# Kernel tuning notes

Hardware: AMD Instinct MI355X
Metric: run time of the kernel (lower is better)

## Reference

```python
import jax, jax.numpy as jnp
import numpy as np

B, M, N_DIM = 2048, 1024, 64


def setup_inputs() -> dict:
    key = jax.random.key(0)
    ks = jax.random.split(key, 6)
    X = jax.random.normal(ks[0], (B, N_DIM), dtype=jnp.float32)
    Mu0 = jax.random.normal(ks[1], (M, N_DIM), dtype=jnp.float32)
    Mu1 = jax.random.normal(ks[2], (M, N_DIM), dtype=jnp.float32)
    # diagonal variances must be positive
    S0 = jax.random.uniform(ks[3], (M, N_DIM), dtype=jnp.float32, minval=0.1, maxval=1.0)
    S1 = jax.random.uniform(ks[4], (M, N_DIM), dtype=jnp.float32, minval=0.1, maxval=1.0)
    Lam = jax.random.uniform(ks[5], (M,), dtype=jnp.float32, minval=0.01, maxval=1.0)
    Lam = Lam / jnp.sum(Lam)  # transport-plan weights sum to 1
    return {"X": X, "Mu0": Mu0, "Mu1": Mu1, "S0": S0, "S1": S1,
            "Lam": Lam, "t": 0.3, "epsilon": 0.5}


def reference(X, Mu0, Mu1, S0, S1, Lam, t, epsilon):
    # GMMflow_fast.calc_u with sparse coupling of M nonzero (i,j) pairs.
    eps2 = epsilon ** 2
    Ds = jnp.sqrt(4.0 * S0 * S1 + epsilon ** 4)            # [M, n]
    Cs = 0.5 * (Ds - eps2)                                  # [M, n]
    v = Mu1 - Mu0                                           # [M, n]
    Mut = (1.0 - t) * Mu0 + t * Mu1                         # [M, n]
    Sigma = ((1.0 - t) ** 2) * S0 + (t ** 2) * S1 + 2.0 * t * (1.0 - t) * (Cs + 0.5 * eps2)
    Pt = t * S1 + (1.0 - t) * Cs
    Qt = (1.0 - t) * S0 + t * Cs
    St = Pt - Qt - eps2 * t
    K = St / Sigma                                          # [M, n]

    Xd = X[:, None, :] - Mut[None, :, :]                    # [B, M, n]
    U = K[None, :, :] * Xd + v[None, :, :]                  # [B, M, n]

    # Gaussian log-prob plus (n/2) log(2*pi), matching the torch code:
    # log N(x; mu, Sigma) + n/2 log(2pi) = -0.5 * sum(d^2/Sigma + log Sigma)
    logw = -0.5 * jnp.sum(Xd * Xd / Sigma[None, :, :] + jnp.log(Sigma)[None, :, :], axis=-1)  # [B, M]
    logw = jnp.clip(logw, -50.0, 50.0)
    W = jnp.exp(logw) * Lam[None, :]                        # [B, M]

    u = jnp.einsum('bm,bmd->bd', W, U)                      # [B, n]
    norm = jnp.sum(W, axis=1, keepdims=True)                # [B, 1]
    return u / norm
```

## Files before the change

kernel.cpp:

```cpp
#include <hip/hip_runtime.h>
#include <math.h>


#define B_N 2048
#define M_N 1024
#define NSPLIT 16
#define BT 64
#define MS 64
#define PROW 132

typedef short bf16x8 __attribute__((ext_vector_type(8)));
typedef float f32x4 __attribute__((ext_vector_type(4)));

static __device__ __forceinline__ unsigned short bf16rn(float f) {
    union { float f; unsigned u; } v; v.f = f;
    unsigned r = v.u + 0x7FFF + ((v.u >> 16) & 1);
    return (unsigned short)(r >> 16);
}
static __device__ __forceinline__ float bf2f(unsigned short h) {
    union { unsigned u; float f; } v; v.u = ((unsigned)h) << 16;
    return v.f;
}
static __device__ __forceinline__ void st4(unsigned short* p, unsigned short a,
                                           unsigned short b, unsigned short c, unsigned short d) {
    union { unsigned short u[4]; float2 f; } t;
    t.u[0] = a; t.u[1] = b; t.u[2] = c; t.u[3] = d;
    *(float2*)p = t.f;
}

__global__ __launch_bounds__(256)
void prep_kernel(const float* __restrict__ Mu0, const float* __restrict__ Mu1,
                 const float* __restrict__ S0, const float* __restrict__ S1,
                 const float* __restrict__ T, const float* __restrict__ E,
                 unsigned short* __restrict__ B1h, unsigned short* __restrict__ B1l,
                 unsigned short* __restrict__ VTh, float* __restrict__ qArr) {
    __shared__ float sK[16 * 65];
    __shared__ float sG[16 * 65];
    const int tid = threadIdx.x;
    const int m0 = blockIdx.x * 16;
    const float t = T[0], e = E[0];
    const float eps2 = e * e, eps4 = eps2 * eps2, omt = 1.f - t;
    const int d = tid & 63;
    #pragma unroll
    for (int it = 0; it < 4; it++) {
        int mi = it * 4 + (tid >> 6);
        int m = m0 + mi;
        int idx = m * 64 + d;
        float s0 = S0[idx], s1 = S1[idx];
        float mu0 = Mu0[idx], mu1 = Mu1[idx];
        float Ds = sqrtf(4.f * s0 * s1 + eps4);
        float Cs = 0.5f * (Ds - eps2);
        float sig = omt * omt * s0 + t * t * s1 + 2.f * t * omt * (Cs + 0.5f * eps2);
        float St = (t * s1 + omt * Cs) - (omt * s0 + t * Cs) - eps2 * t;
        float a = 1.f / sig;
        float K = St * a;
        float mut = omt * mu0 + t * mu1;
        float pp = -2.f * mut * a;
        float g = (mu1 - mu0) - K * mut;
        unsigned short ah = bf16rn(a);
        B1h[m * 128 + d] = ah;
        B1l[m * 128 + d] = bf16rn(a - bf2f(ah));
        unsigned short ph = bf16rn(pp);
        B1h[m * 128 + 64 + d] = ph;
        B1l[m * 128 + 64 + d] = bf16rn(pp - bf2f(ph));
        sK[mi * 65 + d] = K;
        sG[mi * 65 + d] = g;
        float qd = mut * mut * a + logf(sig);
        #pragma unroll
        for (int off = 32; off > 0; off >>= 1) qd += __shfl_xor(qd, off, 64);
        if (d == 0) qArr[m] = qd;
    }
    __syncthreads();
    #pragma unroll
    for (int it = 0; it < 8; it++) {
        int i = it * 256 + tid;
        int n = i >> 4, mm = i & 15;
        float v = (n < 64) ? sK[mm * 65 + n] : sG[mm * 65 + (n - 64)];
        VTh[n * M_N + m0 + mm] = bf16rn(v);
    }
}

__global__ __launch_bounds__(256, 2)
void gmm_main_kernel(const float* __restrict__ X, const float* __restrict__ Lam,
                     const unsigned short* __restrict__ B1h, const unsigned short* __restrict__ B1l,
                     const unsigned short* __restrict__ VTh,
                     const float* __restrict__ qArr, float* __restrict__ part) {
    __shared__ __align__(16) char smem_raw[70144];
    unsigned short* sm = (unsigned short*)smem_raw;
    unsigned short* sA1h = sm;
    unsigned short* sA1l = sm + 8704;
    unsigned short* sB1h = sm + 17408;
    unsigned short* sB1l = sm + 26112;
    unsigned short* sV   = sm;
    unsigned short* sW   = sm + 17408;
    float* sQ = (float*)(smem_raw + 69632);
    float* sL = (float*)(smem_raw + 69888);

    const int tid  = threadIdx.x;
    const int Boff = blockIdx.x * BT;
    const int Moff = blockIdx.y * MS;
    const int w    = tid >> 6;
    const int lane = tid & 63;
    const int c = lane & 15, q = lane >> 4;
    const int wb = w >> 1;
    const int wm = w & 1;

    {
        const float4* X4 = (const float4*)X;
        #pragma unroll
        for (int it = 0; it < 4; it++) {
            int i = it * 256 + tid;
            int b = i >> 4, dq = i & 15;
            float4 xv = X4[(size_t)(Boff + b) * 16 + dq];
            float xs[4] = {xv.x, xv.y, xv.z, xv.w};
            unsigned short yh[4], yl[4], xh[4], xl[4];
            #pragma unroll
            for (int k = 0; k < 4; k++) {
                float y = xs[k] * xs[k];
                yh[k] = bf16rn(y);  yl[k] = bf16rn(y - bf2f(yh[k]));
                xh[k] = bf16rn(xs[k]);  xl[k] = bf16rn(xs[k] - bf2f(xh[k]));
            }
            int base = b * 136 + 4 * dq;
            st4(sA1h + base, yh[0], yh[1], yh[2], yh[3]);
            st4(sA1l + base, yl[0], yl[1], yl[2], yl[3]);
            st4(sA1h + base + 64, xh[0], xh[1], xh[2], xh[3]);
            st4(sA1l + base + 64, xl[0], xl[1], xl[2], xl[3]);
        }
        const float4* gBh = (const float4*)B1h + (size_t)Moff * 16;
        const float4* gBl = (const float4*)B1l + (size_t)Moff * 16;
        #pragma unroll
        for (int it = 0; it < 4; it++) {
            int i = it * 256 + tid;
            int row = i >> 4, cc = i & 15;
            *(float4*)(sB1h + row * 136 + cc * 8) = gBh[row * 16 + cc];
            *(float4*)(sB1l + row * 136 + cc * 8) = gBl[row * 16 + cc];
        }
        if (tid < 64) sQ[tid] = qArr[Moff + tid];
        else if (tid < 128) sL[tid - 64] = Lam[Moff + tid - 64];
    }
    __syncthreads();

    f32x4 acc1[2][2];
    #pragma unroll
    for (int i = 0; i < 2; i++)
        #pragma unroll
        for (int j = 0; j < 2; j++) acc1[i][j] = (f32x4){0.f, 0.f, 0.f, 0.f};
    #pragma unroll
    for (int ks = 0; ks < 4; ks++) {
        bf16x8 Ah[2], Al[2], Bh[2], Bl[2];
        #pragma unroll
        for (int i = 0; i < 2; i++) {
            int row = wb * 32 + i * 16 + c;
            Ah[i] = *(const bf16x8*)(sA1h + row * 136 + ks * 32 + q * 8);
            Al[i] = *(const bf16x8*)(sA1l + row * 136 + ks * 32 + q * 8);
        }
        #pragma unroll
        for (int j = 0; j < 2; j++) {
            int row = wm * 32 + j * 16 + c;
            Bh[j] = *(const bf16x8*)(sB1h + row * 136 + ks * 32 + q * 8);
            Bl[j] = *(const bf16x8*)(sB1l + row * 136 + ks * 32 + q * 8);
        }
        #pragma unroll
        for (int i = 0; i < 2; i++)
            #pragma unroll
            for (int j = 0; j < 2; j++) {
                acc1[i][j] = __builtin_amdgcn_mfma_f32_16x16x32_bf16(Ah[i], Bh[j], acc1[i][j], 0, 0, 0);
                acc1[i][j] = __builtin_amdgcn_mfma_f32_16x16x32_bf16(Ah[i], Bl[j], acc1[i][j], 0, 0, 0);
                acc1[i][j] = __builtin_amdgcn_mfma_f32_16x16x32_bf16(Al[i], Bh[j], acc1[i][j], 0, 0, 0);
            }
    }
    __syncthreads();

    {
        const float4* gV = (const float4*)VTh;
        int mo8 = Moff >> 3;
        #pragma unroll
        for (int it = 0; it < 4; it++) {
            int i = it * 256 + tid;
            int row = i >> 3, cc = i & 7;
            *(float4*)(sV + row * 72 + cc * 8) = gV[(size_t)row * 128 + mo8 + cc];
        }
        float nsum[2][4];
        #pragma unroll
        for (int i = 0; i < 2; i++)
            #pragma unroll
            for (int r = 0; r < 4; r++) nsum[i][r] = 0.f;
        #pragma unroll
        for (int i = 0; i < 2; i++)
            #pragma unroll
            for (int j = 0; j < 2; j++) {
                int m = wm * 32 + j * 16 + c;
                float qm = sQ[m], lm = sL[m];
                #pragma unroll
                for (int r = 0; r < 4; r++) {
                    int bl = wb * 32 + i * 16 + q * 4 + r;
                    float lw = -0.5f * (acc1[i][j][r] + qm);
                    lw = fminf(50.f, fmaxf(-50.f, lw));
                    float wf = __expf(lw) * lm;
                    unsigned short wh = bf16rn(wf);
                    sW[bl * 72 + m] = wh;
                    nsum[i][r] += bf2f(wh);
                }
            }
        #pragma unroll
        for (int mask = 1; mask <= 8; mask <<= 1)
            #pragma unroll
            for (int i = 0; i < 2; i++)
                #pragma unroll
                for (int r = 0; r < 4; r++)
                    nsum[i][r] += __shfl_xor(nsum[i][r], mask, 64);
        if (c == 0) {
            #pragma unroll
            for (int i = 0; i < 2; i++)
                #pragma unroll
                for (int r = 0; r < 4; r++) {
                    int b = Boff + wb * 32 + i * 16 + q * 4 + r;
                    part[((size_t)blockIdx.y * B_N + b) * PROW + 128 + wm] = nsum[i][r];
                }
        }
    }
    __syncthreads();

    f32x4 acc2[2][4];
    #pragma unroll
    for (int i = 0; i < 2; i++)
        #pragma unroll
        for (int j = 0; j < 4; j++) acc2[i][j] = (f32x4){0.f, 0.f, 0.f, 0.f};
    #pragma unroll
    for (int ks = 0; ks < 2; ks++) {
        bf16x8 Wf[2], Vf[4];
        #pragma unroll
        for (int i = 0; i < 2; i++) {
            int row = wb * 32 + i * 16 + c;
            Wf[i] = *(const bf16x8*)(sW + row * 72 + ks * 32 + q * 8);
        }
        #pragma unroll
        for (int j = 0; j < 4; j++) {
            int row = wm * 64 + j * 16 + c;
            Vf[j] = *(const bf16x8*)(sV + row * 72 + ks * 32 + q * 8);
        }
        #pragma unroll
        for (int i = 0; i < 2; i++)
            #pragma unroll
            for (int j = 0; j < 4; j++)
                acc2[i][j] = __builtin_amdgcn_mfma_f32_16x16x32_bf16(Wf[i], Vf[j], acc2[i][j], 0, 0, 0);
    }

    #pragma unroll
    for (int i = 0; i < 2; i++)
        #pragma unroll
        for (int j = 0; j < 4; j++) {
            #pragma unroll
            for (int r = 0; r < 4; r++) {
                int b = Boff + wb * 32 + i * 16 + q * 4 + r;
                int n = wm * 64 + j * 16 + c;
                part[((size_t)blockIdx.y * B_N + b) * PROW + n] = acc2[i][j][r];
            }
        }
}

__global__ __launch_bounds__(256)
void finalize_kernel(const float* __restrict__ X, const float* __restrict__ part,
                     float* __restrict__ out) {
    int gid = blockIdx.x * 256 + threadIdx.x;
    int b = gid >> 6, d = gid & 63;
    float a1 = 0.f, a2 = 0.f, nn = 0.f;
    #pragma unroll
    for (int s = 0; s < NSPLIT; s++) {
        const float* row = part + ((size_t)s * B_N + b) * PROW;
        a1 += row[d];
        a2 += row[64 + d];
        nn += row[128] + row[129];
    }
    out[gid] = (X[gid] * a1 + a2) / nn;
}

extern "C" void kernel_launch(void* const* d_in, const int* in_sizes, int n_in,
                              void* d_out, int out_size, void* d_ws, size_t ws_size,
                              hipStream_t stream) {
    (void)in_sizes; (void)n_in; (void)out_size; (void)ws_size;
    const float* X   = (const float*)d_in[0];
    const float* Mu0 = (const float*)d_in[1];
    const float* Mu1 = (const float*)d_in[2];
    const float* S0  = (const float*)d_in[3];
    const float* S1  = (const float*)d_in[4];
    const float* Lam = (const float*)d_in[5];
    const float* T   = (const float*)d_in[6];
    const float* E   = (const float*)d_in[7];

    char* ws = (char*)d_ws;
    unsigned short* B1h = (unsigned short*)(ws);
    unsigned short* B1l = (unsigned short*)(ws + 262144);
    unsigned short* VTh = (unsigned short*)(ws + 524288);
    float* qArr = (float*)(ws + 786432);
    float* part = (float*)(ws + 790528);

    prep_kernel<<<64, 256, 0, stream>>>(Mu0, Mu1, S0, S1, T, E, B1h, B1l, VTh, qArr);
    dim3 grid(B_N / BT, NSPLIT);
    gmm_main_kernel<<<grid, 256, 0, stream>>>(X, Lam, B1h, B1l, VTh, qArr, part);
    finalize_kernel<<<512, 256, 0, stream>>>(X, part, (float*)d_out);
}
```

Baseline: 90.08 us.

## Fuse prep and finalize into main kernel with last-block reduction

The separate prep kernel is removed: each main-kernel block now recomputes its slice of per-component coefficients (B1 hi/lo, K/g, q) directly into shared memory and registers. The finalize kernel is also removed. Instead, an atomic counter per batch tile lets the last-arriving split block sum the partials and write the output. This cuts two launches and the global round trips for the intermediates. In exchange, coefficient work is repeated across the 32 batch tiles, register pressure rises from the kg array, and a memset plus atomics are added.

```diff
diff --git a/kernel.cpp b/kernel.cpp
--- a/kernel.cpp
+++ b/kernel.cpp
@@ -28,64 +28,15 @@
     *(float2*)p = t.f;
 }
 
-__global__ __launch_bounds__(256)
-void prep_kernel(const float* __restrict__ Mu0, const float* __restrict__ Mu1,
-                 const float* __restrict__ S0, const float* __restrict__ S1,
-                 const float* __restrict__ T, const float* __restrict__ E,
-                 unsigned short* __restrict__ B1h, unsigned short* __restrict__ B1l,
-                 unsigned short* __restrict__ VTh, float* __restrict__ qArr) {
-    __shared__ float sK[16 * 65];
-    __shared__ float sG[16 * 65];
-    const int tid = threadIdx.x;
-    const int m0 = blockIdx.x * 16;
-    const float t = T[0], e = E[0];
-    const float eps2 = e * e, eps4 = eps2 * eps2, omt = 1.f - t;
-    const int d = tid & 63;
-    #pragma unroll
-    for (int it = 0; it < 4; it++) {
-        int mi = it * 4 + (tid >> 6);
-        int m = m0 + mi;
-        int idx = m * 64 + d;
-        float s0 = S0[idx], s1 = S1[idx];
-        float mu0 = Mu0[idx], mu1 = Mu1[idx];
-        float Ds = sqrtf(4.f * s0 * s1 + eps4);
-        float Cs = 0.5f * (Ds - eps2);
-        float sig = omt * omt * s0 + t * t * s1 + 2.f * t * omt * (Cs + 0.5f * eps2);
-        float St = (t * s1 + omt * Cs) - (omt * s0 + t * Cs) - eps2 * t;
-        float a = 1.f / sig;
-        float K = St * a;
-        float mut = omt * mu0 + t * mu1;
-        float pp = -2.f * mut * a;
-        float g = (mu1 - mu0) - K * mut;
-        unsigned short ah = bf16rn(a);
-        B1h[m * 128 + d] = ah;
-        B1l[m * 128 + d] = bf16rn(a - bf2f(ah));
-        unsigned short ph = bf16rn(pp);
-        B1h[m * 128 + 64 + d] = ph;
-        B1l[m * 128 + 64 + d] = bf16rn(pp - bf2f(ph));
-        sK[mi * 65 + d] = K;
-        sG[mi * 65 + d] = g;
-        float qd = mut * mut * a + logf(sig);
-        #pragma unroll
-        for (int off = 32; off > 0; off >>= 1) qd += __shfl_xor(qd, off, 64);
-        if (d == 0) qArr[m] = qd;
-    }
-    __syncthreads();
-    #pragma unroll
-    for (int it = 0; it < 8; it++) {
-        int i = it * 256 + tid;
-        int n = i >> 4, mm = i & 15;
-        float v = (n < 64) ? sK[mm * 65 + n] : sG[mm * 65 + (n - 64)];
-        VTh[n * M_N + m0 + mm] = bf16rn(v);
-    }
-}
-
 __global__ __launch_bounds__(256, 2)
-void gmm_main_kernel(const float* __restrict__ X, const float* __restrict__ Lam,
-                     const unsigned short* __restrict__ B1h, const unsigned short* __restrict__ B1l,
-                     const unsigned short* __restrict__ VTh,
-                     const float* __restrict__ qArr, float* __restrict__ part) {
-    __shared__ __align__(16) char smem_raw[70144];
+void gmm_main_kernel(const float* __restrict__ X,
+                     const float* __restrict__ Mu0, const float* __restrict__ Mu1,
+                     const float* __restrict__ S0, const float* __restrict__ S1,
+                     const float* __restrict__ Lam,
+                     const float* __restrict__ T, const float* __restrict__ E,
+                     float* __restrict__ part, int* __restrict__ cnt,
+                     float* __restrict__ out) {
+    __shared__ __align__(16) char smem_raw[70400];
     unsigned short* sm = (unsigned short*)smem_raw;
     unsigned short* sA1h = sm;
     unsigned short* sA1l = sm + 8704;
@@ -95,6 +46,7 @@
     unsigned short* sW   = sm + 17408;
     float* sQ = (float*)(smem_raw + 69632);
     float* sL = (float*)(smem_raw + 69888);
+    int*  sWin = (int*)(smem_raw + 70144);
 
     const int tid  = threadIdx.x;
     const int Boff = blockIdx.x * BT;
@@ -104,14 +56,49 @@
     const int c = lane & 15, q = lane >> 4;
     const int wb = w >> 1;
     const int wm = w & 1;
-
+    const int d  = lane;
+    const int mq = tid >> 6;
+
+    ushort2 kg[16];
+    {
+        const float t = T[0], e = E[0];
+        const float eps2 = e * e, eps4 = eps2 * eps2, omt = 1.f - t;
+        #pragma unroll 4
+        for (int it = 0; it < 16; it++) {
+            int mloc = it * 4 + mq;
+            int idx = (Moff + mloc) * 64 + d;
+            float s0 = S0[idx], s1 = S1[idx];
+            float mu0 = Mu0[idx], mu1 = Mu1[idx];
+            float Ds = sqrtf(4.f * s0 * s1 + eps4);
+            float Cs = 0.5f * (Ds - eps2);
+            float sig = omt * omt * s0 + t * t * s1 + 2.f * t * omt * (Cs + 0.5f * eps2);
+            float St = (t * s1 + omt * Cs) - (omt * s0 + t * Cs) - eps2 * t;
+            float a = 1.f / sig;
+            float K = St * a;
+            float mut = omt * mu0 + t * mu1;
+            float pp = -2.f * mut * a;
+            float g = (mu1 - mu0) - K * mut;
+            unsigned short ah = bf16rn(a);
+            sB1h[mloc * 136 + d] = ah;
+            sB1l[mloc * 136 + d] = bf16rn(a - bf2f(ah));
+            unsigned short ph = bf16rn(pp);
+            sB1h[mloc * 136 + 64 + d] = ph;
+            sB1l[mloc * 136 + 64 + d] = bf16rn(pp - bf2f(ph));
+            kg[it] = make_ushort2(bf16rn(K), bf16rn(g));
+            float qd = mut * mut * a + __logf(sig);
+            #pragma unroll
+            for (int off = 32; off > 0; off >>= 1) qd += __shfl_xor(qd, off, 64);
+            if (d == 0) sQ[mloc] = qd;
+        }
+        if (tid < 64) sL[tid] = Lam[Moff + tid];
+    }
     {
         const float4* X4 = (const float4*)X;
         #pragma unroll
         for (int it = 0; it < 4; it++) {
             int i = it * 256 + tid;
-            int b = i >> 4, dq = i & 15;
-            float4 xv = X4[(size_t)(Boff + b) * 16 + dq];
+            int b = i >> 4, dq4 = i & 15;
+            float4 xv = X4[(size_t)(Boff + b) * 16 + dq4];
             float xs[4] = {xv.x, xv.y, xv.z, xv.w};
             unsigned short yh[4], yl[4], xh[4], xl[4];
             #pragma unroll
@@ -120,23 +107,12 @@
                 yh[k] = bf16rn(y);  yl[k] = bf16rn(y - bf2f(yh[k]));
                 xh[k] = bf16rn(xs[k]);  xl[k] = bf16rn(xs[k] - bf2f(xh[k]));
             }
-            int base = b * 136 + 4 * dq;
+            int base = b * 136 + 4 * dq4;
             st4(sA1h + base, yh[0], yh[1], yh[2], yh[3]);
             st4(sA1l + base, yl[0], yl[1], yl[2], yl[3]);
             st4(sA1h + base + 64, xh[0], xh[1], xh[2], xh[3]);
             st4(sA1l + base + 64, xl[0], xl[1], xl[2], xl[3]);
         }
-        const float4* gBh = (const float4*)B1h + (size_t)Moff * 16;
-        const float4* gBl = (const float4*)B1l + (size_t)Moff * 16;
-        #pragma unroll
-        for (int it = 0; it < 4; it++) {
-            int i = it * 256 + tid;
-            int row = i >> 4, cc = i & 15;
-            *(float4*)(sB1h + row * 136 + cc * 8) = gBh[row * 16 + cc];
-            *(float4*)(sB1l + row * 136 + cc * 8) = gBl[row * 16 + cc];
-        }
-        if (tid < 64) sQ[tid] = qArr[Moff + tid];
-        else if (tid < 128) sL[tid - 64] = Lam[Moff + tid - 64];
     }
     __syncthreads();
 
@@ -172,13 +148,11 @@
     __syncthreads();
 
     {
-        const float4* gV = (const float4*)VTh;
-        int mo8 = Moff >> 3;
-        #pragma unroll
-        for (int it = 0; it < 4; it++) {
-            int i = it * 256 + tid;
-            int row = i >> 3, cc = i & 7;
-            *(float4*)(sV + row * 72 + cc * 8) = gV[(size_t)row * 128 + mo8 + cc];
+        #pragma unroll 4
+        for (int it = 0; it < 16; it++) {
+            int mloc = it * 4 + mq;
+            sV[d * 72 + mloc]        = kg[it].x;
+            sV[(64 + d) * 72 + mloc] = kg[it].y;
         }
         float nsum[2][4];
         #pragma unroll
@@ -257,22 +231,48 @@
                 part[((size_t)blockIdx.y * B_N + b) * PROW + n] = acc2[i][j][r];
             }
         }
-}
-
-__global__ __launch_bounds__(256)
-void finalize_kernel(const float* __restrict__ X, const float* __restrict__ part,
-                     float* __restrict__ out) {
-    int gid = blockIdx.x * 256 + threadIdx.x;
-    int b = gid >> 6, d = gid & 63;
-    float a1 = 0.f, a2 = 0.f, nn = 0.f;
-    #pragma unroll
-    for (int s = 0; s < NSPLIT; s++) {
-        const float* row = part + ((size_t)s * B_N + b) * PROW;
-        a1 += row[d];
-        a2 += row[64 + d];
-        nn += row[128] + row[129];
-    }
-    out[gid] = (X[gid] * a1 + a2) / nn;
+
+    __syncthreads();
+    if (tid == 0) {
+        __threadfence();
+        int old = atomicAdd(&cnt[blockIdx.x], 1);
+        *sWin = (old == NSPLIT - 1);
+    }
+    __syncthreads();
+    if (!*sWin) return;
+    __threadfence();
+
+    {
+        int b = Boff + (tid >> 2);
+        int d0 = (tid & 3) * 16;
+        float a1[16], a2[16], nn = 0.f;
+        #pragma unroll
+        for (int k = 0; k < 16; k++) { a1[k] = 0.f; a2[k] = 0.f; }
+        for (int s = 0; s < NSPLIT; s++) {
+            const float* row = part + ((size_t)s * B_N + b) * PROW;
+            #pragma unroll
+            for (int k = 0; k < 4; k++) {
+                float4 v1 = *(const float4*)(row + d0 + 4 * k);
+                float4 v2 = *(const float4*)(row + 64 + d0 + 4 * k);
+                a1[4 * k] += v1.x; a1[4 * k + 1] += v1.y; a1[4 * k + 2] += v1.z; a1[4 * k + 3] += v1.w;
+                a2[4 * k] += v2.x; a2[4 * k + 1] += v2.y; a2[4 * k + 2] += v2.z; a2[4 * k + 3] += v2.w;
+            }
+            nn += row[128] + row[129];
+        }
+        float rn = 1.f / nn;
+        const float4* X4 = (const float4*)(X + (size_t)b * 64 + d0);
+        float4* O4 = (float4*)(out + (size_t)b * 64 + d0);
+        #pragma unroll
+        for (int k = 0; k < 4; k++) {
+            float4 xv = X4[k];
+            float4 o;
+            o.x = (xv.x * a1[4 * k]     + a2[4 * k])     * rn;
+            o.y = (xv.y * a1[4 * k + 1] + a2[4 * k + 1]) * rn;
+            o.z = (xv.z * a1[4 * k + 2] + a2[4 * k + 2]) * rn;
+            o.w = (xv.w * a1[4 * k + 3] + a2[4 * k + 3]) * rn;
+            O4[k] = o;
+        }
+    }
 }
 
 extern "C" void kernel_launch(void* const* d_in, const int* in_sizes, int n_in,
@@ -289,14 +289,11 @@
     const float* E   = (const float*)d_in[7];
 
     char* ws = (char*)d_ws;
-    unsigned short* B1h = (unsigned short*)(ws);
-    unsigned short* B1l = (unsigned short*)(ws + 262144);
-    unsigned short* VTh = (unsigned short*)(ws + 524288);
-    float* qArr = (float*)(ws + 786432);
-    float* part = (float*)(ws + 790528);
-
-    prep_kernel<<<64, 256, 0, stream>>>(Mu0, Mu1, S0, S1, T, E, B1h, B1l, VTh, qArr);
+    int*   cnt  = (int*)ws;
+    float* part = (float*)(ws + 256);
+
+    hipMemsetAsync(cnt, 0, 128, stream);
     dim3 grid(B_N / BT, NSPLIT);
-    gmm_main_kernel<<<grid, 256, 0, stream>>>(X, Lam, B1h, B1l, VTh, qArr, part);
-    finalize_kernel<<<512, 256, 0, stream>>>(X, part, (float*)d_out);
-}
+    gmm_main_kernel<<<grid, 256, 0, stream>>>(X, Mu0, Mu1, S0, S1, Lam, T, E,
+                                              part, cnt, (float*)d_out);
+}
```

Result: slower. 124.9 us (+38.7%).

## Store split-M partials as bf16, vectorize finalize, widen prep grid

Applied to the files above, without the earlier changes.

The main kernel now writes its per-split numerator partials as bf16 into a dense 128-wide array, with the normalizer sums in a separate float array, instead of a padded fp32 132-wide array. This roughly halves partial-sum write and read traffic between the main and finalize kernels. Finalize now uses 4-wide vector loads and stores and a reciprocal multiply. Prep runs on 256 blocks of 4 rows instead of 64 blocks of 16 and uses fast __logf. Rounding the partials to bf16 before summing 16 splits adds precision error to the output.

```diff
diff --git a/kernel.cpp b/kernel.cpp
--- a/kernel.cpp
+++ b/kernel.cpp
@@ -7,7 +7,6 @@
 #define NSPLIT 16
 #define BT 64
 #define MS 64
-#define PROW 132
 
 typedef short bf16x8 __attribute__((ext_vector_type(8)));
 typedef float f32x4 __attribute__((ext_vector_type(4)));
@@ -34,47 +33,43 @@
                  const float* __restrict__ T, const float* __restrict__ E,
                  unsigned short* __restrict__ B1h, unsigned short* __restrict__ B1l,
                  unsigned short* __restrict__ VTh, float* __restrict__ qArr) {
-    __shared__ float sK[16 * 65];
-    __shared__ float sG[16 * 65];
+    __shared__ float sK[4 * 65];
+    __shared__ float sG[4 * 65];
     const int tid = threadIdx.x;
-    const int m0 = blockIdx.x * 16;
+    const int m0 = blockIdx.x * 4;
+    const int mi = tid >> 6, d = tid & 63;
+    const int m = m0 + mi;
     const float t = T[0], e = E[0];
     const float eps2 = e * e, eps4 = eps2 * eps2, omt = 1.f - t;
-    const int d = tid & 63;
-    #pragma unroll
-    for (int it = 0; it < 4; it++) {
-        int mi = it * 4 + (tid >> 6);
-        int m = m0 + mi;
-        int idx = m * 64 + d;
-        float s0 = S0[idx], s1 = S1[idx];
-        float mu0 = Mu0[idx], mu1 = Mu1[idx];
-        float Ds = sqrtf(4.f * s0 * s1 + eps4);
-        float Cs = 0.5f * (Ds - eps2);
-        float sig = omt * omt * s0 + t * t * s1 + 2.f * t * omt * (Cs + 0.5f * eps2);
-        float St = (t * s1 + omt * Cs) - (omt * s0 + t * Cs) - eps2 * t;
-        float a = 1.f / sig;
-        float K = St * a;
-        float mut = omt * mu0 + t * mu1;
-        float pp = -2.f * mut * a;
-        float g = (mu1 - mu0) - K * mut;
-        unsigned short ah = bf16rn(a);
-        B1h[m * 128 + d] = ah;
-        B1l[m * 128 + d] = bf16rn(a - bf2f(ah));
-        unsigned short ph = bf16rn(pp);
-        B1h[m * 128 + 64 + d] = ph;
-        B1l[m * 128 + 64 + d] = bf16rn(pp - bf2f(ph));
-        sK[mi * 65 + d] = K;
-        sG[mi * 65 + d] = g;
-        float qd = mut * mut * a + logf(sig);
-        #pragma unroll
-        for (int off = 32; off > 0; off >>= 1) qd += __shfl_xor(qd, off, 64);
-        if (d == 0) qArr[m] = qd;
-    }
+    int idx = m * 64 + d;
+    float s0 = S0[idx], s1 = S1[idx];
+    float mu0 = Mu0[idx], mu1 = Mu1[idx];
+    float Ds = sqrtf(4.f * s0 * s1 + eps4);
+    float Cs = 0.5f * (Ds - eps2);
+    float sig = omt * omt * s0 + t * t * s1 + 2.f * t * omt * (Cs + 0.5f * eps2);
+    float St = (t * s1 + omt * Cs) - (omt * s0 + t * Cs) - eps2 * t;
+    float a = 1.f / sig;
+    float K = St * a;
+    float mut = omt * mu0 + t * mu1;
+    float pp = -2.f * mut * a;
+    float g = (mu1 - mu0) - K * mut;
+    unsigned short ah = bf16rn(a);
+    B1h[m * 128 + d] = ah;
+    B1l[m * 128 + d] = bf16rn(a - bf2f(ah));
+    unsigned short ph = bf16rn(pp);
+    B1h[m * 128 + 64 + d] = ph;
+    B1l[m * 128 + 64 + d] = bf16rn(pp - bf2f(ph));
+    sK[mi * 65 + d] = K;
+    sG[mi * 65 + d] = g;
+    float qd = mut * mut * a + __logf(sig);
+    #pragma unroll
+    for (int off = 32; off > 0; off >>= 1) qd += __shfl_xor(qd, off, 64);
+    if (d == 0) qArr[m] = qd;
     __syncthreads();
     #pragma unroll
-    for (int it = 0; it < 8; it++) {
+    for (int it = 0; it < 2; it++) {
         int i = it * 256 + tid;
-        int n = i >> 4, mm = i & 15;
+        int n = i >> 2, mm = i & 3;
         float v = (n < 64) ? sK[mm * 65 + n] : sG[mm * 65 + (n - 64)];
         VTh[n * M_N + m0 + mm] = bf16rn(v);
     }
@@ -84,7 +79,8 @@
 void gmm_main_kernel(const float* __restrict__ X, const float* __restrict__ Lam,
                      const unsigned short* __restrict__ B1h, const unsigned short* __restrict__ B1l,
                      const unsigned short* __restrict__ VTh,
-                     const float* __restrict__ qArr, float* __restrict__ part) {
+                     const float* __restrict__ qArr,
+                     unsigned short* __restrict__ partBF, float* __restrict__ partN) {
     __shared__ __align__(16) char smem_raw[70144];
     unsigned short* sm = (unsigned short*)smem_raw;
     unsigned short* sA1h = sm;
@@ -110,8 +106,8 @@
         #pragma unroll
         for (int it = 0; it < 4; it++) {
             int i = it * 256 + tid;
-            int b = i >> 4, dq = i & 15;
-            float4 xv = X4[(size_t)(Boff + b) * 16 + dq];
+            int b = i >> 4, dq4 = i & 15;
+            float4 xv = X4[(size_t)(Boff + b) * 16 + dq4];
             float xs[4] = {xv.x, xv.y, xv.z, xv.w};
             unsigned short yh[4], yl[4], xh[4], xl[4];
             #pragma unroll
@@ -120,7 +116,7 @@
                 yh[k] = bf16rn(y);  yl[k] = bf16rn(y - bf2f(yh[k]));
                 xh[k] = bf16rn(xs[k]);  xl[k] = bf16rn(xs[k] - bf2f(xh[k]));
             }
-            int base = b * 136 + 4 * dq;
+            int base = b * 136 + 4 * dq4;
             st4(sA1h + base, yh[0], yh[1], yh[2], yh[3]);
             st4(sA1l + base, yl[0], yl[1], yl[2], yl[3]);
             st4(sA1h + base + 64, xh[0], xh[1], xh[2], xh[3]);
@@ -215,7 +211,7 @@
                 #pragma unroll
                 for (int r = 0; r < 4; r++) {
                     int b = Boff + wb * 32 + i * 16 + q * 4 + r;
-                    part[((size_t)blockIdx.y * B_N + b) * PROW + 128 + wm] = nsum[i][r];
+                    partN[((size_t)blockIdx.y * B_N + b) * 2 + wm] = nsum[i][r];
                 }
         }
     }
@@ -254,25 +250,35 @@
             for (int r = 0; r < 4; r++) {
                 int b = Boff + wb * 32 + i * 16 + q * 4 + r;
                 int n = wm * 64 + j * 16 + c;
-                part[((size_t)blockIdx.y * B_N + b) * PROW + n] = acc2[i][j][r];
+                partBF[((size_t)blockIdx.y * B_N + b) * 128 + n] = bf16rn(acc2[i][j][r]);
             }
         }
 }
 
-__global__ __launch_bounds__(256)
-void finalize_kernel(const float* __restrict__ X, const float* __restrict__ part,
-                     float* __restrict__ out) {
-    int gid = blockIdx.x * 256 + threadIdx.x;
-    int b = gid >> 6, d = gid & 63;
-    float a1 = 0.f, a2 = 0.f, nn = 0.f;
+__global__ __launch_bounds__(128)
+void finalize_kernel(const float* __restrict__ X, const unsigned short* __restrict__ partBF,
+                     const float* __restrict__ partN, float* __restrict__ out) {
+    int gid = blockIdx.x * 128 + threadIdx.x;
+    int b = gid >> 4, d0 = (gid & 15) * 4;
+    float a1[4] = {0.f, 0.f, 0.f, 0.f}, a2[4] = {0.f, 0.f, 0.f, 0.f}, nn = 0.f;
     #pragma unroll
     for (int s = 0; s < NSPLIT; s++) {
-        const float* row = part + ((size_t)s * B_N + b) * PROW;
-        a1 += row[d];
-        a2 += row[64 + d];
-        nn += row[128] + row[129];
-    }
-    out[gid] = (X[gid] * a1 + a2) / nn;
+        const unsigned short* row = partBF + ((size_t)s * B_N + b) * 128;
+        ushort4 v1 = *(const ushort4*)(row + d0);
+        ushort4 v2 = *(const ushort4*)(row + 64 + d0);
+        a1[0] += bf2f(v1.x); a1[1] += bf2f(v1.y); a1[2] += bf2f(v1.z); a1[3] += bf2f(v1.w);
+        a2[0] += bf2f(v2.x); a2[1] += bf2f(v2.y); a2[2] += bf2f(v2.z); a2[3] += bf2f(v2.w);
+        float2 nv = *(const float2*)(partN + ((size_t)s * B_N + b) * 2);
+        nn += nv.x + nv.y;
+    }
+    float rn = 1.f / nn;
+    float4 xv = *(const float4*)(X + (size_t)b * 64 + d0);
+    float4 o;
+    o.x = (xv.x * a1[0] + a2[0]) * rn;
+    o.y = (xv.y * a1[1] + a2[1]) * rn;
+    o.z = (xv.z * a1[2] + a2[2]) * rn;
+    o.w = (xv.w * a1[3] + a2[3]) * rn;
+    *(float4*)(out + (size_t)b * 64 + d0) = o;
 }
 
 extern "C" void kernel_launch(void* const* d_in, const int* in_sizes, int n_in,
@@ -289,14 +295,15 @@
     const float* E   = (const float*)d_in[7];
 
     char* ws = (char*)d_ws;
-    unsigned short* B1h = (unsigned short*)(ws);
-    unsigned short* B1l = (unsigned short*)(ws + 262144);
-    unsigned short* VTh = (unsigned short*)(ws + 524288);
-    float* qArr = (float*)(ws + 786432);
-    float* part = (float*)(ws + 790528);
-
-    prep_kernel<<<64, 256, 0, stream>>>(Mu0, Mu1, S0, S1, T, E, B1h, B1l, VTh, qArr);
+    unsigned short* B1h   = (unsigned short*)(ws);
+    unsigned short* B1l   = (unsigned short*)(ws + 262144);
+    unsigned short* VTh   = (unsigned short*)(ws + 524288);
+    float*          qArr  = (float*)(ws + 786432);
+    unsigned short* partBF= (unsigned short*)(ws + 790528);
+    float*          partN = (float*)(ws + 790528 + 8388608);
+
+    prep_kernel<<<256, 256, 0, stream>>>(Mu0, Mu1, S0, S1, T, E, B1h, B1l, VTh, qArr);
     dim3 grid(B_N / BT, NSPLIT);
-    gmm_main_kernel<<<grid, 256, 0, stream>>>(X, Lam, B1h, B1l, VTh, qArr, part);
-    finalize_kernel<<<512, 256, 0, stream>>>(X, part, (float*)d_out);
-}
+    gmm_main_kernel<<<grid, 256, 0, stream>>>(X, Lam, B1h, B1l, VTh, qArr, partBF, partN);
+    finalize_kernel<<<256, 128, 0, stream>>>(X, partBF, partN, (float*)d_out);
+}
```

New measurement: 83.21 us (median of 2 runs). -7.6%, faster.
